# Kernel optimization log

Hardware: AMD Instinct MI355X
Metric: run time of the kernel (lower is better)

## Reference

```python
import jax, jax.numpy as jnp
import numpy as np

B, S, H = 8, 512, 768
NH, KVH, HD = 12, 4, 64
E, TOPK, IE = 8, 2, 1536
EPS = 1e-6
ROPE_THETA = 10000.0


def _rmsnorm(x, w):
    xf = x.astype(jnp.float32)
    var = jnp.mean(xf * xf, axis=-1, keepdims=True)
    return (w * (xf * jax.lax.rsqrt(var + EPS))).astype(x.dtype)


def _rotate_half(x):
    x1, x2 = jnp.split(x, 2, axis=-1)
    return jnp.concatenate((-x2, x1), axis=-1)


def setup_inputs() -> dict:
    key = jax.random.key(0)
    ks = iter(jax.random.split(key, 40))

    def nrm(shape, scale=0.02):
        return jax.random.normal(next(ks), shape, dtype=jnp.float32) * scale

    inp = {}
    inp["hidden_states"] = jax.random.normal(next(ks), (B, S, H), dtype=jnp.float32)
    causal = jnp.tril(jnp.ones((S, S), dtype=bool))
    inp["attention_mask"] = jnp.where(causal, 0.0, -1e9).astype(jnp.float32)[None, None]  # [1,1,S,S]
    inp["group_attention_mask"] = jnp.zeros((S, 1, B, B), dtype=jnp.float32)
    inp["position_ids"] = jnp.broadcast_to(jnp.arange(S, dtype=jnp.int32), (B, S))
    # RMSNorm weights
    inp["ln1_w"] = jnp.ones((H,), jnp.float32)
    inp["ln2_w"] = jnp.ones((H,), jnp.float32)
    inp["ln3_w"] = jnp.ones((H,), jnp.float32)
    # self (time) attention params
    inp["sq_w"] = nrm((NH * HD, H)); inp["sq_b"] = jnp.zeros((NH * HD,), jnp.float32)
    inp["sk_w"] = nrm((KVH * HD, H)); inp["sk_b"] = jnp.zeros((KVH * HD,), jnp.float32)
    inp["sv_w"] = nrm((KVH * HD, H)); inp["sv_b"] = jnp.zeros((KVH * HD,), jnp.float32)
    inp["so_w"] = nrm((H, NH * HD))
    # group (cross-channel) attention params
    inp["gq_w"] = nrm((NH * HD, H)); inp["gq_b"] = jnp.zeros((NH * HD,), jnp.float32)
    inp["gk_w"] = nrm((KVH * HD, H)); inp["gk_b"] = jnp.zeros((KVH * HD,), jnp.float32)
    inp["gv_w"] = nrm((KVH * HD, H)); inp["gv_b"] = jnp.zeros((KVH * HD,), jnp.float32)
    inp["go_w"] = nrm((H, NH * HD))
    # MoE params: router + stacked expert weights
    inp["gate_w"] = nrm((E, H))
    inp["w_gate"] = nrm((E, H, IE))
    inp["w_up"] = nrm((E, H, IE))
    inp["w_down"] = nrm((E, IE, H))
    return inp


def reference(hidden_states, attention_mask, group_attention_mask, position_ids,
              ln1_w, ln2_w, ln3_w,
              sq_w, sq_b, sk_w, sk_b, sv_w, sv_b, so_w,
              gq_w, gq_b, gk_w, gk_b, gv_w, gv_b, go_w,
              gate_w, w_gate, w_up, w_down):
    dtype = hidden_states.dtype
    b, s, h = hidden_states.shape
    rep = NH // KVH
    scale = 1.0 / np.sqrt(HD).astype(np.float32)

    # ---- self attention with RoPE (causal, GQA) ----
    residual = hidden_states
    x = _rmsnorm(hidden_states, ln1_w)
    q = (x @ sq_w.T + sq_b).reshape(b, s, NH, HD).transpose(0, 2, 1, 3)   # [b,n,s,d]
    k = (x @ sk_w.T + sk_b).reshape(b, s, KVH, HD).transpose(0, 2, 1, 3)
    v = (x @ sv_w.T + sv_b).reshape(b, s, KVH, HD).transpose(0, 2, 1, 3)
    inv_freq = 1.0 / (ROPE_THETA ** (jnp.arange(0, HD, 2, dtype=jnp.float32) / HD))
    freqs = position_ids.astype(jnp.float32)[..., None] * inv_freq        # [b,s,d/2]
    emb = jnp.concatenate((freqs, freqs), axis=-1)
    cos = jnp.cos(emb)[:, None].astype(dtype)                             # [b,1,s,d]
    sin = jnp.sin(emb)[:, None].astype(dtype)
    q = q * cos + _rotate_half(q) * sin
    k = k * cos + _rotate_half(k) * sin
    k = jnp.repeat(k, rep, axis=1)
    v = jnp.repeat(v, rep, axis=1)
    scores = jnp.einsum('bnqd,bnkd->bnqk', q, k) * scale + attention_mask
    probs = jax.nn.softmax(scores.astype(jnp.float32), axis=-1).astype(dtype)
    attn = jnp.einsum('bnqk,bnkd->bnqd', probs, v)
    attn = attn.transpose(0, 2, 1, 3).reshape(b, s, h) @ so_w.T
    hidden_states = residual + attn

    # ---- group attention: MHA across channels (batch dim), no RoPE ----
    residual = hidden_states
    xg = _rmsnorm(hidden_states, ln2_w).transpose(1, 0, 2)                # [s,b,h]
    q = (xg @ gq_w.T + gq_b).reshape(s, b, NH, HD).transpose(0, 2, 1, 3)  # [s,n,b,d]
    k = (xg @ gk_w.T + gk_b).reshape(s, b, KVH, HD).transpose(0, 2, 1, 3)
    v = (xg @ gv_w.T + gv_b).reshape(s, b, KVH, HD).transpose(0, 2, 1, 3)
    k = jnp.repeat(k, rep, axis=1)
    v = jnp.repeat(v, rep, axis=1)
    gsc = jnp.einsum('snbd,sncd->snbc', q, k) * scale + group_attention_mask
    gpr = jax.nn.softmax(gsc.astype(jnp.float32), axis=-1).astype(dtype)
    ga = jnp.einsum('snbc,sncd->snbd', gpr, v)                            # [s,n,b,d]
    ga = ga.transpose(0, 2, 1, 3).reshape(s, b, h) @ go_w.T               # [s,b,h]
    hidden_states = residual + ga.transpose(1, 0, 2)

    # ---- sparse MoE FFN (top-k routing, weights NOT renormalized) ----
    residual = hidden_states
    xf = _rmsnorm(hidden_states, ln3_w).reshape(b * s, h)                 # [T,h]
    logits = xf @ gate_w.T                                                # [T,E]
    routing = jax.nn.softmax(logits.astype(jnp.float32), axis=-1)
    topw, topi = jax.lax.top_k(routing, TOPK)
    combine = jnp.zeros((b * s, E), jnp.float32).at[
        jnp.arange(b * s)[:, None], topi].set(topw)                        # [T,E]
    out = jnp.zeros_like(xf)
    for e in range(E):  # fixed small expert count; each iter is a grouped GEMM
        ge = jax.nn.silu(xf @ w_gate[e]) * (xf @ w_up[e])                 # [T,IE]
        out = out + combine[:, e:e + 1].astype(dtype) * (ge @ w_down[e])
    hidden_states = residual + out.reshape(b, s, h)
    return hidden_states
```

## Files before the change

### kernel.cpp

```cpp
#include <hip/hip_runtime.h>
#include <math.h>

#define BATCH 8
#define SEQ 512
#define HID 768
#define NHEAD 12
#define KVHEAD 4
#define HDIM 64
#define NEXP 8
#define TOPK 2
#define IEXP 1536
#define NTOK (BATCH * SEQ)
#define NSLOT (NTOK * TOPK)
#define REP (NHEAD / KVHEAD)

typedef unsigned short u16;
typedef float f32x4 __attribute__((ext_vector_type(4)));
typedef __bf16 bf16x8 __attribute__((ext_vector_type(8)));
typedef unsigned short u16x8 __attribute__((ext_vector_type(8)));

__device__ __forceinline__ u16 f2bf(float f) {
    unsigned u = __float_as_uint(f);
    u += 0x7fffu + ((u >> 16) & 1u);
    return (u16)(u >> 16);
}
__device__ __forceinline__ float bf2f(u16 h) {
    return __uint_as_float(((unsigned)h) << 16);
}

__device__ __forceinline__ void gload16(const void* g, void* l) {
    __builtin_amdgcn_global_load_lds(
        (const __attribute__((address_space(1))) void*)g,
        (__attribute__((address_space(3))) void*)l, 16, 0, 0);
}

__device__ __forceinline__ void cvt8(float4 a, float4 b, u16x8& hi, u16x8& lo) {
    float x[8] = {a.x, a.y, a.z, a.w, b.x, b.y, b.z, b.w};
#pragma unroll
    for (int i = 0; i < 8; ++i) {
        u16 h = f2bf(x[i]);
        hi[i] = h;
        lo[i] = f2bf(x[i] - bf2f(h));
    }
}

#define SW(row, col) (((row) << 6) + ((col) ^ (((row) & 7) << 3)))

__global__ __launch_bounds__(256)
void cvt_split(const float* __restrict__ x, u16* __restrict__ yh,
               u16* __restrict__ yl, int n) {
    int i = (blockIdx.x * 256 + threadIdx.x) * 4;
    if (i >= n) return;
    float4 v = *(const float4*)(x + i);
    float a[4] = {v.x, v.y, v.z, v.w};
    ushort4 h, lo;
    u16 t;
    t = f2bf(a[0]); h.x = t; lo.x = f2bf(a[0] - bf2f(t));
    t = f2bf(a[1]); h.y = t; lo.y = f2bf(a[1] - bf2f(t));
    t = f2bf(a[2]); h.z = t; lo.z = f2bf(a[2] - bf2f(t));
    t = f2bf(a[3]); h.w = t; lo.w = f2bf(a[3] - bf2f(t));
    *(ushort4*)(yh + i) = h;
    *(ushort4*)(yl + i) = lo;
}

__global__ __launch_bounds__(256)
void transpose_cvt(const float* __restrict__ src, u16* __restrict__ dst,
                   int R, int C) {
    const int e = blockIdx.z;
    src += (size_t)e * R * C;
    dst += (size_t)e * R * C;
    __shared__ float t[32][33];
    const int c0 = blockIdx.x << 5, r0 = blockIdx.y << 5;
    const int tx = threadIdx.x, ty = threadIdx.y;
#pragma unroll
    for (int i = 0; i < 4; ++i)
        t[ty * 4 + i][tx] = src[(size_t)(r0 + ty * 4 + i) * C + c0 + tx];
    __syncthreads();
#pragma unroll
    for (int i = 0; i < 4; ++i)
        dst[(size_t)(c0 + ty * 4 + i) * R + r0 + tx] = f2bf(t[tx][ty * 4 + i]);
}

__global__ __launch_bounds__(256)
void rmsnorm_kernel(const float* __restrict__ X, const float* __restrict__ W,
                    float* __restrict__ Y) {
    const int t = blockIdx.x;
    const int tid = threadIdx.x;
    const float* x = X + (size_t)t * HID;
    float x0 = x[tid], x1 = x[tid + 256], x2 = x[tid + 512];
    float ss = x0 * x0 + x1 * x1 + x2 * x2;
    for (int m = 1; m < 64; m <<= 1) ss += __shfl_xor(ss, m);
    __shared__ float red[4];
    if ((tid & 63) == 0) red[tid >> 6] = ss;
    __syncthreads();
    float tot = red[0] + red[1] + red[2] + red[3];
    float inv = rsqrtf(tot * (1.0f / HID) + 1e-6f);
    float* y = Y + (size_t)t * HID;
    y[tid]       = x0 * inv * W[tid];
    y[tid + 256] = x1 * inv * W[tid + 256];
    y[tid + 512] = x2 * inv * W[tid + 512];
}

__global__ __launch_bounds__(256)
void qkv_split(const float* __restrict__ X, const u16* __restrict__ Wh,
               const u16* __restrict__ Wl,
               const float* __restrict__ bq, const float* __restrict__ bk,
               const float* __restrict__ bv,
               float* __restrict__ Qo, float* __restrict__ Ko,
               float* __restrict__ Vo) {
    __shared__ __align__(16) u16 Ah[4096], Al[4096], Bh[4096], Bl[4096];
    const int tid = threadIdx.x, l = tid & 63, w = tid >> 6;
    const int wm = w & 1, wn = w >> 1;
    const int m0 = blockIdx.y << 7, n0 = blockIdx.x << 7;
    const int sr = l >> 2, sc8 = (l & 3) << 3;
    const float* gA0 = X + (size_t)(m0 + w * 32 + sr) * HID + sc8;
    const float* gA1 = gA0 + 16 * HID;
    const u16* gBh0 = Wh + (size_t)(n0 + w * 32 + sr) * HID + sc8;
    const u16* gBh1 = gBh0 + 16 * HID;
    const u16* gBl0 = Wl + (size_t)(n0 + w * 32 + sr) * HID + sc8;
    const u16* gBl1 = gBl0 + 16 * HID;
    const int aoff0 = (w * 32 + sr) * 32 + sc8, aoff1 = aoff0 + 512;
    u16* lBh0 = Bh + w * 1024; u16* lBh1 = lBh0 + 512;
    u16* lBl0 = Bl + w * 1024; u16* lBl1 = lBl0 + 512;
    const int fr = l & 15, fc = (l >> 4) << 3;
    f32x4 acc[4][4];
#pragma unroll
    for (int i = 0; i < 4; ++i)
#pragma unroll
        for (int j = 0; j < 4; ++j) acc[i][j] = (f32x4){0.f, 0.f, 0.f, 0.f};
    for (int k0 = 0; k0 < HID; k0 += 32) {
        float4 a00 = *(const float4*)(gA0 + k0);
        float4 a01 = *(const float4*)(gA0 + k0 + 4);
        float4 a10 = *(const float4*)(gA1 + k0);
        float4 a11 = *(const float4*)(gA1 + k0 + 4);
        gload16(gBh0 + k0, lBh0);
        gload16(gBh1 + k0, lBh1);
        gload16(gBl0 + k0, lBl0);
        gload16(gBl1 + k0, lBl1);
        u16x8 h0, l0v, h1, l1v;
        cvt8(a00, a01, h0, l0v);
        cvt8(a10, a11, h1, l1v);
        *(u16x8*)(Ah + aoff0) = h0; *(u16x8*)(Al + aoff0) = l0v;
        *(u16x8*)(Ah + aoff1) = h1; *(u16x8*)(Al + aoff1) = l1v;
        __syncthreads();
        bf16x8 ah[4], al[4], bh[4], bl[4];
#pragma unroll
        for (int i = 0; i < 4; ++i) {
            ah[i] = *(const bf16x8*)(Ah + (wm * 64 + i * 16 + fr) * 32 + fc);
            al[i] = *(const bf16x8*)(Al + (wm * 64 + i * 16 + fr) * 32 + fc);
            bh[i] = *(const bf16x8*)(Bh + (wn * 64 + i * 16 + fr) * 32 + fc);
            bl[i] = *(const bf16x8*)(Bl + (wn * 64 + i * 16 + fr) * 32 + fc);
        }
#pragma unroll
        for (int mf = 0; mf < 4; ++mf)
#pragma unroll
            for (int nf = 0; nf < 4; ++nf) {
                acc[mf][nf] = __builtin_amdgcn_mfma_f32_16x16x32_bf16(
                    ah[mf], bh[nf], acc[mf][nf], 0, 0, 0);
                acc[mf][nf] = __builtin_amdgcn_mfma_f32_16x16x32_bf16(
                    al[mf], bh[nf], acc[mf][nf], 0, 0, 0);
                acc[mf][nf] = __builtin_amdgcn_mfma_f32_16x16x32_bf16(
                    ah[mf], bl[nf], acc[mf][nf], 0, 0, 0);
            }
        __syncthreads();
    }
    float* outp; const float* bp; int ldc, nl;
    if (n0 < 768)       { outp = Qo; bp = bq; ldc = 768; nl = n0; }
    else if (n0 < 1024) { outp = Ko; bp = bk; ldc = 256; nl = n0 - 768; }
    else                { outp = Vo; bp = bv; ldc = 256; nl = n0 - 1024; }
    const int er = (l >> 4) << 2, ec = l & 15;
#pragma unroll
    for (int mf = 0; mf < 4; ++mf)
#pragma unroll
        for (int i = 0; i < 4; ++i) {
            int row = m0 + wm * 64 + mf * 16 + er + i;
#pragma unroll
            for (int nf = 0; nf < 4; ++nf) {
                int col = nl + wn * 64 + nf * 16 + ec;
                outp[(size_t)row * ldc + col] = acc[mf][nf][i] + bp[col];
            }
        }
}

__global__ __launch_bounds__(256)
void oproj_split(const float* __restrict__ A, const u16* __restrict__ Wh,
                 const u16* __restrict__ Wl, const float* __restrict__ resid,
                 float* __restrict__ C, int M, int N, int K) {
    __shared__ __align__(16) u16 Ah[4096], Al[4096], Bh[4096], Bl[4096];
    const int tid = threadIdx.x, l = tid & 63, w = tid >> 6;
    const int wm = w & 1, wn = w >> 1;
    const int m0 = blockIdx.y << 7, n0 = blockIdx.x << 7;
    const int sr = l >> 2, sc8 = (l & 3) << 3;
    const float* gA0 = A + (size_t)(m0 + w * 32 + sr) * K + sc8;
    const float* gA1 = gA0 + (size_t)16 * K;
    const u16* gBh0 = Wh + (size_t)(n0 + w * 32 + sr) * K + sc8;
    const u16* gBh1 = gBh0 + (size_t)16 * K;
    const u16* gBl0 = Wl + (size_t)(n0 + w * 32 + sr) * K + sc8;
    const u16* gBl1 = gBl0 + (size_t)16 * K;
    const int aoff0 = (w * 32 + sr) * 32 + sc8, aoff1 = aoff0 + 512;
    u16* lBh0 = Bh + w * 1024; u16* lBh1 = lBh0 + 512;
    u16* lBl0 = Bl + w * 1024; u16* lBl1 = lBl0 + 512;
    const int fr = l & 15, fc = (l >> 4) << 3;
    f32x4 acc[4][4];
#pragma unroll
    for (int i = 0; i < 4; ++i)
#pragma unroll
        for (int j = 0; j < 4; ++j) acc[i][j] = (f32x4){0.f, 0.f, 0.f, 0.f};
    for (int k0 = 0; k0 < K; k0 += 32) {
        float4 a00 = *(const float4*)(gA0 + k0);
        float4 a01 = *(const float4*)(gA0 + k0 + 4);
        float4 a10 = *(const float4*)(gA1 + k0);
        float4 a11 = *(const float4*)(gA1 + k0 + 4);
        gload16(gBh0 + k0, lBh0);
        gload16(gBh1 + k0, lBh1);
        gload16(gBl0 + k0, lBl0);
        gload16(gBl1 + k0, lBl1);
        u16x8 h0, l0v, h1, l1v;
        cvt8(a00, a01, h0, l0v);
        cvt8(a10, a11, h1, l1v);
        *(u16x8*)(Ah + aoff0) = h0; *(u16x8*)(Al + aoff0) = l0v;
        *(u16x8*)(Ah + aoff1) = h1; *(u16x8*)(Al + aoff1) = l1v;
        __syncthreads();
        bf16x8 ah[4], al[4], bh[4], bl[4];
#pragma unroll
        for (int i = 0; i < 4; ++i) {
            ah[i] = *(const bf16x8*)(Ah + (wm * 64 + i * 16 + fr) * 32 + fc);
            al[i] = *(const bf16x8*)(Al + (wm * 64 + i * 16 + fr) * 32 + fc);
            bh[i] = *(const bf16x8*)(Bh + (wn * 64 + i * 16 + fr) * 32 + fc);
            bl[i] = *(const bf16x8*)(Bl + (wn * 64 + i * 16 + fr) * 32 + fc);
        }
#pragma unroll
        for (int mf = 0; mf < 4; ++mf)
#pragma unroll
            for (int nf = 0; nf < 4; ++nf) {
                acc[mf][nf] = __builtin_amdgcn_mfma_f32_16x16x32_bf16(
                    ah[mf], bh[nf], acc[mf][nf], 0, 0, 0);
                acc[mf][nf] = __builtin_amdgcn_mfma_f32_16x16x32_bf16(
                    al[mf], bh[nf], acc[mf][nf], 0, 0, 0);
                acc[mf][nf] = __builtin_amdgcn_mfma_f32_16x16x32_bf16(
                    ah[mf], bl[nf], acc[mf][nf], 0, 0, 0);
            }
        __syncthreads();
    }
    const int er = (l >> 4) << 2, ec = l & 15;
#pragma unroll
    for (int mf = 0; mf < 4; ++mf)
#pragma unroll
        for (int i = 0; i < 4; ++i) {
            int row = m0 + wm * 64 + mf * 16 + er + i;
#pragma unroll
            for (int nf = 0; nf < 4; ++nf) {
                int col = n0 + wn * 64 + nf * 16 + ec;
                C[(size_t)row * N + col] =
                    acc[mf][nf][i] + resid[(size_t)row * N + col];
            }
        }
}

__global__ __launch_bounds__(256)
void rope_kernel(float* __restrict__ Q, float* __restrict__ Kb,
                 const int* __restrict__ pos_ids) {
    const int t = blockIdx.x;
    const float pos = (float)pos_ids[t];
    const int tid = threadIdx.x;
#pragma unroll
    for (int it = 0; it < 2; ++it) {
        int p = tid + (it << 8);
        int head = p >> 5, i = p & 31;
        float invf = expf(-(float)i * 0.28782313662425572f);
        float ang = pos * invf;
        float c = cosf(ang), sn = sinf(ang);
        float* base = (head < NHEAD)
            ? (Q + (size_t)t * HID + head * HDIM)
            : (Kb + (size_t)t * (KVHEAD * HDIM) + (head - NHEAD) * HDIM);
        float x1 = base[i], x2 = base[i + 32];
        base[i]      = x1 * c - x2 * sn;
        base[i + 32] = x2 * c + x1 * sn;
    }
}

__global__ __launch_bounds__(256)
void attn_self_mfma(const float* __restrict__ Q, const float* __restrict__ K,
                    const float* __restrict__ V, float* __restrict__ O) {
    const int qt = blockIdx.x, n = blockIdx.y, b = blockIdx.z;
    const int kv = n / REP;
    const int tid = threadIdx.x, l = tid & 63, w = tid >> 6;
    const int q0 = qt << 5;
    __shared__ __align__(16) u16 Qh[2048], Ql[2048];
    __shared__ __align__(16) u16 Kh[4096], Kl[4096];
    __shared__ __align__(16) u16 Vh[4096], Vl[4096];
    __shared__ float Ps[32][68];
    __shared__ float scal[32];

    {
        int row = tid >> 3, cg = (tid & 7) << 3;
        const float* qg = Q + (size_t)(b * SEQ + q0 + row) * HID + n * HDIM + cg;
        float4 v0 = *(const float4*)qg;
        float4 v1 = *(const float4*)(qg + 4);
        u16x8 h, lo;
        cvt8(v0, v1, h, lo);
        *(u16x8*)(Qh + SW(row, cg)) = h;
        *(u16x8*)(Ql + SW(row, cg)) = lo;
    }
    __syncthreads();

    const int fr = l & 15, fcg = (l >> 4) << 3;
    const int qf16 = (w & 1) << 4;
    const int fp2 = (w >> 1) << 1;
    bf16x8 qfh[2], qfl[2];
#pragma unroll
    for (int dc = 0; dc < 2; ++dc) {
        int off = SW(qf16 + fr, dc * 32 + fcg);
        qfh[dc] = *(const bf16x8*)(Qh + off);
        qfl[dc] = *(const bf16x8*)(Ql + off);
    }

    f32x4 o[2];
    o[0] = (f32x4){0.f, 0.f, 0.f, 0.f};
    o[1] = (f32x4){0.f, 0.f, 0.f, 0.f};
    float m_run = -3.4e38f, l_run = 0.f;
    const int sq = tid >> 3;
    const int skb = (tid & 7) << 3;
    const float scale = 0.125f;
    const int nt = (qt >> 1) + 1;

    for (int t = 0; t < nt; ++t) {
        __syncthreads();
        {
            int row = tid >> 2, cg = (tid & 3) << 4;
            const float* kg = K + (size_t)(b * SEQ + (t << 6) + row)
                              * (KVHEAD * HDIM) + kv * HDIM + cg;
            float4 k0 = *(const float4*)kg;
            float4 k1 = *(const float4*)(kg + 4);
            float4 k2 = *(const float4*)(kg + 8);
            float4 k3 = *(const float4*)(kg + 12);
            u16x8 h0, l0v, h1, l1v;
            cvt8(k0, k1, h0, l0v);
            cvt8(k2, k3, h1, l1v);
            *(u16x8*)(Kh + SW(row, cg)) = h0;
            *(u16x8*)(Kh + SW(row, cg + 8)) = h1;
            *(u16x8*)(Kl + SW(row, cg)) = l0v;
            *(u16x8*)(Kl + SW(row, cg + 8)) = l1v;
        }
        {
            int kp = (tid & 31) << 1, dc = (tid >> 5) << 3;
            const float* vg0 = V + (size_t)(b * SEQ + (t << 6) + kp)
                               * (KVHEAD * HDIM) + kv * HDIM + dc;
            const float* vg1 = vg0 + KVHEAD * HDIM;
            float4 a0 = *(const float4*)vg0;
            float4 a1 = *(const float4*)(vg0 + 4);
            float4 b0 = *(const float4*)vg1;
            float4 b1 = *(const float4*)(vg1 + 4);
            float va[8] = {a0.x, a0.y, a0.z, a0.w, a1.x, a1.y, a1.z, a1.w};
            float vb[8] = {b0.x, b0.y, b0.z, b0.w, b1.x, b1.y, b1.z, b1.w};
#pragma unroll
            for (int j = 0; j < 8; ++j) {
                u16 h0 = f2bf(va[j]);
                u16 h1 = f2bf(vb[j]);
                u16 p0 = f2bf(va[j] - bf2f(h0));
                u16 p1 = f2bf(vb[j] - bf2f(h1));
                int off = SW(dc + j, kp);
                *(unsigned*)(Vh + off) = (unsigned)h0 | ((unsigned)h1 << 16);
                *(unsigned*)(Vl + off) = (unsigned)p0 | ((unsigned)p1 << 16);
            }
        }
        __syncthreads();
#pragma unroll
        for (int kk = 0; kk < 2; ++kk) {
            int kf = fp2 + kk;
            bf16x8 kh[2], klv[2];
#pragma unroll
            for (int dc = 0; dc < 2; ++dc) {
                int off = SW(kf * 16 + fr, dc * 32 + fcg);
                kh[dc]  = *(const bf16x8*)(Kh + off);
                klv[dc] = *(const bf16x8*)(Kl + off);
            }
            f32x4 s = (f32x4){0.f, 0.f, 0.f, 0.f};
            s = __builtin_amdgcn_mfma_f32_16x16x32_bf16(qfh[0], kh[0], s, 0, 0, 0);
            s = __builtin_amdgcn_mfma_f32_16x16x32_bf16(qfh[1], kh[1], s, 0, 0, 0);
            s = __builtin_amdgcn_mfma_f32_16x16x32_bf16(qfl[0], kh[0], s, 0, 0, 0);
            s = __builtin_amdgcn_mfma_f32_16x16x32_bf16(qfl[1], kh[1], s, 0, 0, 0);
            s = __builtin_amdgcn_mfma_f32_16x16x32_bf16(qfh[0], klv[0], s, 0, 0, 0);
            s = __builtin_amdgcn_mfma_f32_16x16x32_bf16(qfh[1], klv[1], s, 0, 0, 0);
            int col = kf * 16 + fr;
            int key = (t << 6) + col;
#pragma unroll
            for (int r = 0; r < 4; ++r) {
                int qrow = qf16 + ((l >> 4) << 2) + r;
                Ps[qrow][col] = (key <= q0 + qrow) ? s[r] * scale : -1e9f;
            }
        }
        __syncthreads();
        {
            float4 s0 = *(const float4*)&Ps[sq][skb];
            float4 s1 = *(const float4*)&Ps[sq][skb + 4];
            float sv[8] = {s0.x, s0.y, s0.z, s0.w, s1.x, s1.y, s1.z, s1.w};
            float mx = sv[0];
#pragma unroll
            for (int j = 1; j < 8; ++j) mx = fmaxf(mx, sv[j]);
            for (int x = 1; x < 8; x <<= 1) mx = fmaxf(mx, __shfl_xor(mx, x));
            float mnew = fmaxf(m_run, mx);
            float corr = __expf(m_run - mnew);
            float lsum = 0.f;
#pragma unroll
            for (int j = 0; j < 8; ++j) {
                sv[j] = __expf(sv[j] - mnew);
                lsum += sv[j];
            }
            for (int x = 1; x < 8; x <<= 1) lsum += __shfl_xor(lsum, x);
            l_run = l_run * corr + lsum;
            m_run = mnew;
            *(float4*)&Ps[sq][skb]     = make_float4(sv[0], sv[1], sv[2], sv[3]);
            *(float4*)&Ps[sq][skb + 4] = make_float4(sv[4], sv[5], sv[6], sv[7]);
            if ((tid & 7) == 0) scal[sq] = corr;
        }
        __syncthreads();
        {
            float4 c4 = *(const float4*)&scal[qf16 + ((l >> 4) << 2)];
            float cr[4] = {c4.x, c4.y, c4.z, c4.w};
#pragma unroll
            for (int dfi = 0; dfi < 2; ++dfi)
#pragma unroll
                for (int r = 0; r < 4; ++r) o[dfi][r] *= cr[r];
            bf16x8 ph[2], pl[2];
#pragma unroll
            for (int kc = 0; kc < 2; ++kc) {
                float4 p0 = *(const float4*)&Ps[qf16 + fr][kc * 32 + fcg];
                float4 p1 = *(const float4*)&Ps[qf16 + fr][kc * 32 + fcg + 4];
                u16x8 hh, ll;
                cvt8(p0, p1, hh, ll);
                ph[kc] = *(bf16x8*)&hh;
                pl[kc] = *(bf16x8*)&ll;
            }
#pragma unroll
            for (int dfi = 0; dfi < 2; ++dfi) {
                int df = fp2 + dfi;
#pragma unroll
                for (int kc = 0; kc < 2; ++kc) {
                    int off = SW(df * 16 + fr, kc * 32 + fcg);
                    bf16x8 vh = *(const bf16x8*)(Vh + off);
                    bf16x8 vl = *(const bf16x8*)(Vl + off);
                    o[dfi] = __builtin_amdgcn_mfma_f32_16x16x32_bf16(
                        ph[kc], vh, o[dfi], 0, 0, 0);
                    o[dfi] = __builtin_amdgcn_mfma_f32_16x16x32_bf16(
                        pl[kc], vh, o[dfi], 0, 0, 0);
                    o[dfi] = __builtin_amdgcn_mfma_f32_16x16x32_bf16(
                        ph[kc], vl, o[dfi], 0, 0, 0);
                }
            }
        }
    }
    __syncthreads();
    if ((tid & 7) == 0) scal[sq] = 1.0f / l_run;
    __syncthreads();
    {
        int qrb = qf16 + ((l >> 4) << 2);
        float4 li4 = *(const float4*)&scal[qrb];
        float li[4] = {li4.x, li4.y, li4.z, li4.w};
#pragma unroll
        for (int dfi = 0; dfi < 2; ++dfi) {
            int df = fp2 + dfi;
            int col = n * HDIM + df * 16 + fr;
#pragma unroll
            for (int r = 0; r < 4; ++r) {
                int row = q0 + qrb + r;
                O[(size_t)(b * SEQ + row) * HID + col] = o[dfi][r] * li[r];
            }
        }
    }
}

__global__ __launch_bounds__(64)
void attn_group(const float* __restrict__ Q, const float* __restrict__ K,
                const float* __restrict__ V, const float* __restrict__ gmask,
                float* __restrict__ O) {
    const int n = blockIdx.x % NHEAD;
    const int s = blockIdx.x / NHEAD;
    const int kv = n / REP;
    const int lane = threadIdx.x;
    __shared__ float Qs[8][65], Ks[8][65], Vs[8][65], Ps[64];
    for (int c = 0; c < 8; ++c) {
        Qs[c][lane] = Q[(size_t)(c * SEQ + s) * HID + n * HDIM + lane];
        Ks[c][lane] = K[(size_t)(c * SEQ + s) * (KVHEAD * HDIM) + kv * HDIM + lane];
        Vs[c][lane] = V[(size_t)(c * SEQ + s) * (KVHEAD * HDIM) + kv * HDIM + lane];
    }
    __syncthreads();
    const int qb = lane >> 3, kb = lane & 7;
    float sc = 0;
    for (int d = 0; d < 64; ++d) sc += Qs[qb][d] * Ks[kb][d];
    sc = sc * 0.125f + gmask[(size_t)s * 64 + qb * 8 + kb];
    float m = sc;
    for (int x = 1; x < 8; x <<= 1) m = fmaxf(m, __shfl_xor(m, x));
    float p = __expf(sc - m);
    float l = p;
    for (int x = 1; x < 8; x <<= 1) l += __shfl_xor(l, x);
    Ps[lane] = p / l;
    __syncthreads();
    for (int q2 = 0; q2 < 8; ++q2) {
        float o = 0;
        for (int c = 0; c < 8; ++c) o += Ps[q2 * 8 + c] * Vs[c][lane];
        O[(size_t)(q2 * SEQ + s) * HID + n * HDIM + lane] = o;
    }
}

__global__ __launch_bounds__(64)
void router_kernel(const float* __restrict__ X, const float* __restrict__ GW,
                   int* __restrict__ counts, int* __restrict__ topi,
                   float* __restrict__ topw, int* __restrict__ posb) {
    const int t = blockIdx.x;
    const int lane = threadIdx.x;
    const int e = lane >> 3, c = lane & 7;
    const float4* x4 = (const float4*)(X + (size_t)t * HID + c * 96);
    const float4* g4 = (const float4*)(GW + (size_t)e * HID + c * 96);
    float p = 0;
#pragma unroll
    for (int i = 0; i < 24; ++i) {
        float4 xv = x4[i], gv = g4[i];
        p += xv.x * gv.x + xv.y * gv.y + xv.z * gv.z + xv.w * gv.w;
    }
    p += __shfl_xor(p, 1);
    p += __shfl_xor(p, 2);
    p += __shfl_xor(p, 4);
    float lg[8];
#pragma unroll
    for (int i = 0; i < 8; ++i) lg[i] = __shfl(p, i * 8);
    float m = lg[0];
#pragma unroll
    for (int i = 1; i < 8; ++i) m = fmaxf(m, lg[i]);
    float s = 0;
#pragma unroll
    for (int i = 0; i < 8; ++i) { lg[i] = expf(lg[i] - m); s += lg[i]; }
    float inv = 1.0f / s;
    int i1 = 0; float b1 = lg[0];
#pragma unroll
    for (int i = 1; i < 8; ++i) if (lg[i] > b1) { b1 = lg[i]; i1 = i; }
    int i2 = -1; float b2 = -1.0f;
#pragma unroll
    for (int i = 0; i < 8; ++i)
        if (i != i1 && lg[i] > b2) { b2 = lg[i]; i2 = i; }
    if (lane == 0) {
        topi[t * 2] = i1; topi[t * 2 + 1] = i2;
        topw[t * 2] = b1 * inv; topw[t * 2 + 1] = b2 * inv;
        posb[t * 2] = atomicAdd(&counts[i1], 1);
        posb[t * 2 + 1] = atomicAdd(&counts[i2], 1);
    }
}

__global__ void scan_kernel(const int* __restrict__ counts, int* __restrict__ offsets) {
    int acc = 0;
    for (int e = 0; e < NEXP; ++e) { offsets[e] = acc; acc += counts[e]; }
}

__global__ __launch_bounds__(256)
void fill_slots(const int* __restrict__ topi, const float* __restrict__ topw,
                const int* __restrict__ posb, const int* __restrict__ offsets,
                int* __restrict__ slot_token, float* __restrict__ slot_w,
                int* __restrict__ token_slot) {
    int t = blockIdx.x * 256 + threadIdx.x;
    if (t >= NTOK) return;
#pragma unroll
    for (int k = 0; k < TOPK; ++k) {
        int e = topi[t * 2 + k];
        int sl = offsets[e] + posb[t * 2 + k];
        slot_token[sl] = t;
        slot_w[sl] = topw[t * 2 + k];
        token_slot[t * 2 + k] = sl;
    }
}

__global__ __launch_bounds__(256)
void moe_gate_up(const float* __restrict__ X, const u16* __restrict__ Wg,
                 const u16* __restrict__ Wu,
                 const int* __restrict__ slot_token,
                 const int* __restrict__ counts,
                 const int* __restrict__ offsets, u16* __restrict__ H) {
    const int e = blockIdx.z;
    const int Ce = counts[e];
    const int m0 = blockIdx.y << 7;
    if (Ce == 0 || m0 >= Ce) return;
    const int n0 = blockIdx.x << 7;
    const int base = offsets[e];
    __shared__ __align__(16) u16 Ah[4096];
    __shared__ __align__(16) u16 Al[4096];
    __shared__ __align__(16) u16 Gs[4096];
    __shared__ __align__(16) u16 Us[4096];
    const int tid = threadIdx.x, l = tid & 63, w = tid >> 6;
    const int wm = w & 1, wn = w >> 1;
    const int sr = l >> 2, sc8 = (l & 3) << 3;
    int r0 = m0 + w * 32 + sr;
    int r1 = r0 + 16;
    int t0 = slot_token[base + min(r0, Ce - 1)];
    int t1 = slot_token[base + min(r1, Ce - 1)];
    const float* gA0 = X + (size_t)t0 * HID + sc8;
    const float* gA1 = X + (size_t)t1 * HID + sc8;
    const u16* Wge = Wg + (size_t)e * IEXP * HID;
    const u16* Wue = Wu + (size_t)e * IEXP * HID;
    const u16* gG0 = Wge + (size_t)(n0 + w * 32 + sr) * HID + sc8;
    const u16* gG1 = gG0 + 16 * HID;
    const u16* gU0 = Wue + (size_t)(n0 + w * 32 + sr) * HID + sc8;
    const u16* gU1 = gU0 + 16 * HID;
    const int aoff0 = (w * 32 + sr) * 32 + sc8, aoff1 = aoff0 + 512;
    u16* lG0 = Gs + w * 1024; u16* lG1 = lG0 + 512;
    u16* lU0 = Us + w * 1024; u16* lU1 = lU0 + 512;
    const int fr = l & 15, fc = (l >> 4) << 3;
    f32x4 accg[4][4], accu[4][4];
#pragma unroll
    for (int i = 0; i < 4; ++i)
#pragma unroll
        for (int j = 0; j < 4; ++j) {
            accg[i][j] = (f32x4){0.f, 0.f, 0.f, 0.f};
            accu[i][j] = (f32x4){0.f, 0.f, 0.f, 0.f};
        }
    for (int k0 = 0; k0 < HID; k0 += 32) {
        float4 a00 = *(const float4*)(gA0 + k0);
        float4 a01 = *(const float4*)(gA0 + k0 + 4);
        float4 a10 = *(const float4*)(gA1 + k0);
        float4 a11 = *(const float4*)(gA1 + k0 + 4);
        gload16(gG0 + k0, lG0);
        gload16(gG1 + k0, lG1);
        gload16(gU0 + k0, lU0);
        gload16(gU1 + k0, lU1);
        u16x8 h0, lo0, h1, lo1;
        cvt8(a00, a01, h0, lo0);
        cvt8(a10, a11, h1, lo1);
        *(u16x8*)(Ah + aoff0) = h0; *(u16x8*)(Al + aoff0) = lo0;
        *(u16x8*)(Ah + aoff1) = h1; *(u16x8*)(Al + aoff1) = lo1;
        __syncthreads();
        bf16x8 ah[4], al[4], gf[4], uf[4];
#pragma unroll
        for (int i = 0; i < 4; ++i) {
            ah[i] = *(const bf16x8*)(Ah + (wm * 64 + i * 16 + fr) * 32 + fc);
            al[i] = *(const bf16x8*)(Al + (wm * 64 + i * 16 + fr) * 32 + fc);
            gf[i] = *(const bf16x8*)(Gs + (wn * 64 + i * 16 + fr) * 32 + fc);
            uf[i] = *(const bf16x8*)(Us + (wn * 64 + i * 16 + fr) * 32 + fc);
        }
#pragma unroll
        for (int mf = 0; mf < 4; ++mf)
#pragma unroll
            for (int nf = 0; nf < 4; ++nf) {
                accg[mf][nf] = __builtin_amdgcn_mfma_f32_16x16x32_bf16(
                    ah[mf], gf[nf], accg[mf][nf], 0, 0, 0);
                accg[mf][nf] = __builtin_amdgcn_mfma_f32_16x16x32_bf16(
                    al[mf], gf[nf], accg[mf][nf], 0, 0, 0);
                accu[mf][nf] = __builtin_amdgcn_mfma_f32_16x16x32_bf16(
                    ah[mf], uf[nf], accu[mf][nf], 0, 0, 0);
                accu[mf][nf] = __builtin_amdgcn_mfma_f32_16x16x32_bf16(
                    al[mf], uf[nf], accu[mf][nf], 0, 0, 0);
            }
        __syncthreads();
    }
    const int er = (l >> 4) << 2, ec = l & 15;
#pragma unroll
    for (int mf = 0; mf < 4; ++mf)
#pragma unroll
        for (int i = 0; i < 4; ++i) {
            int row = m0 + wm * 64 + mf * 16 + er + i;
            if (row >= Ce) continue;
            size_t sl = (size_t)(base + row);
#pragma unroll
            for (int nf = 0; nf < 4; ++nf) {
                int col = n0 + wn * 64 + nf * 16 + ec;
                float g = accg[mf][nf][i];
                float u = accu[mf][nf][i];
                float h = g / (1.0f + __expf(-g)) * u;
                H[sl * IEXP + col] = f2bf(h);
            }
        }
}

__global__ __launch_bounds__(256)
void moe_down_bf16(const u16* __restrict__ Hb, const u16* __restrict__ Wd,
                   const float* __restrict__ slot_w,
                   const int* __restrict__ counts,
                   const int* __restrict__ offsets, float* __restrict__ D) {
    const int e = blockIdx.z;
    const int Ce = counts[e];
    const int m0 = blockIdx.y << 7;
    if (Ce == 0 || m0 >= Ce) return;
    const int n0 = blockIdx.x << 7;
    const int base = offsets[e];
    __shared__ __align__(16) u16 As[4096];
    __shared__ __align__(16) u16 Bs[4096];
    const int tid = threadIdx.x, l = tid & 63, w = tid >> 6;
    const int wm = w & 1, wn = w >> 1;
    const int sr = l >> 2, sc = (l & 3) << 3;
    const u16* Ae = Hb + (size_t)base * IEXP;
    int r0 = min(m0 + w * 32 + sr, Ce - 1);
    int r1 = min(m0 + w * 32 + 16 + sr, Ce - 1);
    const u16* gA0 = Ae + (size_t)r0 * IEXP + sc;
    const u16* gA1 = Ae + (size_t)r1 * IEXP + sc;
    const u16* Wde = Wd + (size_t)e * HID * IEXP;
    const u16* gB0 = Wde + (size_t)(n0 + w * 32 + sr) * IEXP + sc;
    const u16* gB1 = gB0 + 16 * IEXP;
    u16* lA0 = As + w * 1024; u16* lA1 = lA0 + 512;
    u16* lB0 = Bs + w * 1024; u16* lB1 = lB0 + 512;
    const int fr = l & 15, fc = (l >> 4) << 3;
    f32x4 acc[4][4];
#pragma unroll
    for (int i = 0; i < 4; ++i)
#pragma unroll
        for (int j = 0; j < 4; ++j) acc[i][j] = (f32x4){0.f, 0.f, 0.f, 0.f};
    for (int k0 = 0; k0 < IEXP; k0 += 32) {
        gload16(gA0 + k0, lA0);
        gload16(gA1 + k0, lA1);
        gload16(gB0 + k0, lB0);
        gload16(gB1 + k0, lB1);
        __syncthreads();
        bf16x8 af[4], bfv[4];
#pragma unroll
        for (int i = 0; i < 4; ++i) {
            af[i]  = *(const bf16x8*)(As + (wm * 64 + i * 16 + fr) * 32 + fc);
            bfv[i] = *(const bf16x8*)(Bs + (wn * 64 + i * 16 + fr) * 32 + fc);
        }
#pragma unroll
        for (int mf = 0; mf < 4; ++mf)
#pragma unroll
            for (int nf = 0; nf < 4; ++nf)
                acc[mf][nf] = __builtin_amdgcn_mfma_f32_16x16x32_bf16(
                    af[mf], bfv[nf], acc[mf][nf], 0, 0, 0);
        __syncthreads();
    }
    const int er = (l >> 4) << 2, ec = l & 15;
#pragma unroll
    for (int mf = 0; mf < 4; ++mf)
#pragma unroll
        for (int i = 0; i < 4; ++i) {
            int row = m0 + wm * 64 + mf * 16 + er + i;
            if (row >= Ce) continue;
            size_t sl = (size_t)(base + row);
            float sw = slot_w[sl];
#pragma unroll
            for (int nf = 0; nf < 4; ++nf) {
                int col = n0 + wn * 64 + nf * 16 + ec;
                D[sl * HID + col] = acc[mf][nf][i] * sw;
            }
        }
}

__global__ __launch_bounds__(256)
void moe_add(float* __restrict__ out, const float* __restrict__ D,
             const int* __restrict__ token_slot) {
    const int t = blockIdx.y;
    const int h = blockIdx.x * 256 + threadIdx.x;
    int s0 = token_slot[t * 2], s1 = token_slot[t * 2 + 1];
    out[(size_t)t * HID + h] += D[(size_t)s0 * HID + h] + D[(size_t)s1 * HID + h];
}

extern "C" void kernel_launch(void* const* d_in, const int* in_sizes, int n_in,
                              void* d_out, int out_size, void* d_ws, size_t ws_size,
                              hipStream_t stream) {
    const float* hidden = (const float*)d_in[0];
    const float* amask  = (const float*)d_in[1];
    const float* gmask  = (const float*)d_in[2];
    const int*   posids = (const int*)d_in[3];
    const float* ln1 = (const float*)d_in[4];
    const float* ln2 = (const float*)d_in[5];
    const float* ln3 = (const float*)d_in[6];
    const float* sqw = (const float*)d_in[7];  const float* sqb = (const float*)d_in[8];
    const float* skw = (const float*)d_in[9];  const float* skb = (const float*)d_in[10];
    const float* svw = (const float*)d_in[11]; const float* svb = (const float*)d_in[12];
    const float* sow = (const float*)d_in[13];
    const float* gqw = (const float*)d_in[14]; const float* gqb = (const float*)d_in[15];
    const float* gkw = (const float*)d_in[16]; const float* gkb = (const float*)d_in[17];
    const float* gvw = (const float*)d_in[18]; const float* gvb = (const float*)d_in[19];
    const float* gow = (const float*)d_in[20];
    const float* gatew = (const float*)d_in[21];
    const float* wg = (const float*)d_in[22];
    const float* wu = (const float*)d_in[23];
    const float* wd = (const float*)d_in[24];
    float* out = (float*)d_out;
    (void)amask;

    char* base = (char*)d_ws;
    float* xb     = (float*)(base + 0);
    float* qb     = (float*)(base + 12582912);
    float* kbuf   = (float*)(base + 25165824);
    float* vbuf   = (float*)(base + 29360128);
    float* ab     = (float*)(base + 33554432);
    u16* wqkv_sh  = (u16*)(base + 46137344);
    u16* wqkv_sl  = (u16*)(base + 48103424);
    u16* wo_sh    = (u16*)(base + 50069504);
    u16* wo_sl    = (u16*)(base + 51249152);
    u16* wqkv_gh  = (u16*)(base + 52428800);
    u16* wqkv_gl  = (u16*)(base + 54394880);
    u16* wo_gh    = (u16*)(base + 56360960);
    u16* wo_gl    = (u16*)(base + 57540608);
    u16* wgt      = (u16*)(base + 58720256);
    u16* wut      = (u16*)(base + 77594624);
    u16* wdt      = (u16*)(base + 96468992);
    float* slotw  = (float*)(base + 115343360);
    float* topw   = (float*)(base + 115376128);
    int* counts   = (int*)(base + 115408896);
    int* offsets  = (int*)(base + 115409024);
    int* topi     = (int*)(base + 115409408);
    int* posb     = (int*)(base + 115442176);
    int* slot_token = (int*)(base + 115474944);
    int* token_slot = (int*)(base + 115507712);
    u16*   Hbuf  = (u16*)  (base + 12582912);
    float* Dbuf  = (float*)(base + 37748736);

    cvt_split<<<576, 256, 0, stream>>>(sqw, wqkv_sh, wqkv_sl, 589824);
    cvt_split<<<192, 256, 0, stream>>>(skw, wqkv_sh + 589824, wqkv_sl + 589824, 196608);
    cvt_split<<<192, 256, 0, stream>>>(svw, wqkv_sh + 786432, wqkv_sl + 786432, 196608);
    cvt_split<<<576, 256, 0, stream>>>(sow, wo_sh, wo_sl, 589824);
    cvt_split<<<576, 256, 0, stream>>>(gqw, wqkv_gh, wqkv_gl, 589824);
    cvt_split<<<192, 256, 0, stream>>>(gkw, wqkv_gh + 589824, wqkv_gl + 589824, 196608);
    cvt_split<<<192, 256, 0, stream>>>(gvw, wqkv_gh + 786432, wqkv_gl + 786432, 196608);
    cvt_split<<<576, 256, 0, stream>>>(gow, wo_gh, wo_gl, 589824);
    transpose_cvt<<<dim3(48, 24, 8), dim3(32, 8), 0, stream>>>(wg, wgt, HID, IEXP);
    transpose_cvt<<<dim3(48, 24, 8), dim3(32, 8), 0, stream>>>(wu, wut, HID, IEXP);
    transpose_cvt<<<dim3(24, 48, 8), dim3(32, 8), 0, stream>>>(wd, wdt, IEXP, HID);

    rmsnorm_kernel<<<NTOK, 256, 0, stream>>>(hidden, ln1, xb);
    qkv_split<<<dim3(10, 32), 256, 0, stream>>>(xb, wqkv_sh, wqkv_sl,
                                                sqb, skb, svb, qb, kbuf, vbuf);
    rope_kernel<<<NTOK, 256, 0, stream>>>(qb, kbuf, posids);
    attn_self_mfma<<<dim3(SEQ / 32, NHEAD, BATCH), 256, 0, stream>>>(qb, kbuf, vbuf, ab);
    oproj_split<<<dim3(6, 32), 256, 0, stream>>>(ab, wo_sh, wo_sl, hidden, out,
                                                 NTOK, HID, HID);

    rmsnorm_kernel<<<NTOK, 256, 0, stream>>>(out, ln2, xb);
    qkv_split<<<dim3(10, 32), 256, 0, stream>>>(xb, wqkv_gh, wqkv_gl,
                                                gqb, gkb, gvb, qb, kbuf, vbuf);
    attn_group<<<SEQ * NHEAD, 64, 0, stream>>>(qb, kbuf, vbuf, gmask, ab);
    oproj_split<<<dim3(6, 32), 256, 0, stream>>>(ab, wo_gh, wo_gl, out, out,
                                                 NTOK, HID, HID);

    rmsnorm_kernel<<<NTOK, 256, 0, stream>>>(out, ln3, xb);
    hipMemsetAsync(counts, 0, 8 * sizeof(int), stream);
    router_kernel<<<NTOK, 64, 0, stream>>>(xb, gatew, counts, topi, topw, posb);
    scan_kernel<<<1, 1, 0, stream>>>(counts, offsets);
    fill_slots<<<16, 256, 0, stream>>>(topi, topw, posb, offsets,
                                       slot_token, slotw, token_slot);
    moe_gate_up<<<dim3(12, 32, 8), 256, 0, stream>>>(
        xb, wgt, wut, slot_token, counts, offsets, Hbuf);
    moe_down_bf16<<<dim3(6, 32, 8), 256, 0, stream>>>(
        Hbuf, wdt, slotw, counts, offsets, Dbuf);
    moe_add<<<dim3(3, NTOK), 256, 0, stream>>>(out, Dbuf, token_slot);
}
```

Measured before the change: 676.8 us.

## Use single bf16 activations in MoE gate/up and swap grid axes

The final RMSNorm now also writes a bf16 copy of the normalized activations. The MoE gate/up GEMM loads this copy directly into LDS with gload16, replacing the fp32 load, hi/lo split conversion and doubled MFMA count. The error-compensating low half is dropped, which lowers accuracy relative to the split-bf16 path. The grid axes of both MoE GEMMs are also swapped so the token-tile index is the fastest-varying block coordinate, which changes block scheduling order and early-exit behaviour.

Measured after the change: 871.9 us. 28.8% more time.

```diff
diff --git a/kernel.cpp b/kernel.cpp
--- a/kernel.cpp
+++ b/kernel.cpp
@@ -83,7 +83,7 @@
 
 __global__ __launch_bounds__(256)
 void rmsnorm_kernel(const float* __restrict__ X, const float* __restrict__ W,
-                    float* __restrict__ Y) {
+                    float* __restrict__ Y, u16* __restrict__ Ybf) {
     const int t = blockIdx.x;
     const int tid = threadIdx.x;
     const float* x = X + (size_t)t * HID;
@@ -95,10 +95,15 @@
     __syncthreads();
     float tot = red[0] + red[1] + red[2] + red[3];
     float inv = rsqrtf(tot * (1.0f / HID) + 1e-6f);
+    float r0 = x0 * inv * W[tid];
+    float r1 = x1 * inv * W[tid + 256];
+    float r2 = x2 * inv * W[tid + 512];
     float* y = Y + (size_t)t * HID;
-    y[tid]       = x0 * inv * W[tid];
-    y[tid + 256] = x1 * inv * W[tid + 256];
-    y[tid + 512] = x2 * inv * W[tid + 512];
+    y[tid] = r0; y[tid + 256] = r1; y[tid + 512] = r2;
+    if (Ybf) {
+        u16* yb = Ybf + (size_t)t * HID;
+        yb[tid] = f2bf(r0); yb[tid + 256] = f2bf(r1); yb[tid + 512] = f2bf(r2);
+    }
 }
 
 __global__ __launch_bounds__(256)
@@ -569,19 +574,18 @@
 }
 
 __global__ __launch_bounds__(256)
-void moe_gate_up(const float* __restrict__ X, const u16* __restrict__ Wg,
+void moe_gate_up(const u16* __restrict__ Xb, const u16* __restrict__ Wg,
                  const u16* __restrict__ Wu,
                  const int* __restrict__ slot_token,
                  const int* __restrict__ counts,
                  const int* __restrict__ offsets, u16* __restrict__ H) {
     const int e = blockIdx.z;
     const int Ce = counts[e];
-    const int m0 = blockIdx.y << 7;
+    const int m0 = blockIdx.x << 7;
     if (Ce == 0 || m0 >= Ce) return;
-    const int n0 = blockIdx.x << 7;
+    const int n0 = blockIdx.y << 7;
     const int base = offsets[e];
-    __shared__ __align__(16) u16 Ah[4096];
-    __shared__ __align__(16) u16 Al[4096];
+    __shared__ __align__(16) u16 As[4096];
     __shared__ __align__(16) u16 Gs[4096];
     __shared__ __align__(16) u16 Us[4096];
     const int tid = threadIdx.x, l = tid & 63, w = tid >> 6;
@@ -591,15 +595,15 @@
     int r1 = r0 + 16;
     int t0 = slot_token[base + min(r0, Ce - 1)];
     int t1 = slot_token[base + min(r1, Ce - 1)];
-    const float* gA0 = X + (size_t)t0 * HID + sc8;
-    const float* gA1 = X + (size_t)t1 * HID + sc8;
+    const u16* gA0 = Xb + (size_t)t0 * HID + sc8;
+    const u16* gA1 = Xb + (size_t)t1 * HID + sc8;
     const u16* Wge = Wg + (size_t)e * IEXP * HID;
     const u16* Wue = Wu + (size_t)e * IEXP * HID;
     const u16* gG0 = Wge + (size_t)(n0 + w * 32 + sr) * HID + sc8;
     const u16* gG1 = gG0 + 16 * HID;
     const u16* gU0 = Wue + (size_t)(n0 + w * 32 + sr) * HID + sc8;
     const u16* gU1 = gU0 + 16 * HID;
-    const int aoff0 = (w * 32 + sr) * 32 + sc8, aoff1 = aoff0 + 512;
+    u16* lA0 = As + w * 1024; u16* lA1 = lA0 + 512;
     u16* lG0 = Gs + w * 1024; u16* lG1 = lG0 + 512;
     u16* lU0 = Us + w * 1024; u16* lU1 = lU0 + 512;
     const int fr = l & 15, fc = (l >> 4) << 3;
@@ -612,25 +616,17 @@
             accu[i][j] = (f32x4){0.f, 0.f, 0.f, 0.f};
         }
     for (int k0 = 0; k0 < HID; k0 += 32) {
-        float4 a00 = *(const float4*)(gA0 + k0);
-        float4 a01 = *(const float4*)(gA0 + k0 + 4);
-        float4 a10 = *(const float4*)(gA1 + k0);
-        float4 a11 = *(const float4*)(gA1 + k0 + 4);
+        gload16(gA0 + k0, lA0);
+        gload16(gA1 + k0, lA1);
         gload16(gG0 + k0, lG0);
         gload16(gG1 + k0, lG1);
         gload16(gU0 + k0, lU0);
         gload16(gU1 + k0, lU1);
-        u16x8 h0, lo0, h1, lo1;
-        cvt8(a00, a01, h0, lo0);
-        cvt8(a10, a11, h1, lo1);
-        *(u16x8*)(Ah + aoff0) = h0; *(u16x8*)(Al + aoff0) = lo0;
-        *(u16x8*)(Ah + aoff1) = h1; *(u16x8*)(Al + aoff1) = lo1;
-        __syncthreads();
-        bf16x8 ah[4], al[4], gf[4], uf[4];
+        __syncthreads();
+        bf16x8 af[4], gf[4], uf[4];
 #pragma unroll
         for (int i = 0; i < 4; ++i) {
-            ah[i] = *(const bf16x8*)(Ah + (wm * 64 + i * 16 + fr) * 32 + fc);
-            al[i] = *(const bf16x8*)(Al + (wm * 64 + i * 16 + fr) * 32 + fc);
+            af[i] = *(const bf16x8*)(As + (wm * 64 + i * 16 + fr) * 32 + fc);
             gf[i] = *(const bf16x8*)(Gs + (wn * 64 + i * 16 + fr) * 32 + fc);
             uf[i] = *(const bf16x8*)(Us + (wn * 64 + i * 16 + fr) * 32 + fc);
         }
@@ -639,13 +635,9 @@
 #pragma unroll
             for (int nf = 0; nf < 4; ++nf) {
                 accg[mf][nf] = __builtin_amdgcn_mfma_f32_16x16x32_bf16(
-                    ah[mf], gf[nf], accg[mf][nf], 0, 0, 0);
-                accg[mf][nf] = __builtin_amdgcn_mfma_f32_16x16x32_bf16(
-                    al[mf], gf[nf], accg[mf][nf], 0, 0, 0);
+                    af[mf], gf[nf], accg[mf][nf], 0, 0, 0);
                 accu[mf][nf] = __builtin_amdgcn_mfma_f32_16x16x32_bf16(
-                    ah[mf], uf[nf], accu[mf][nf], 0, 0, 0);
-                accu[mf][nf] = __builtin_amdgcn_mfma_f32_16x16x32_bf16(
-                    al[mf], uf[nf], accu[mf][nf], 0, 0, 0);
+                    af[mf], uf[nf], accu[mf][nf], 0, 0, 0);
             }
         __syncthreads();
     }
@@ -675,9 +667,9 @@
                    const int* __restrict__ offsets, float* __restrict__ D) {
     const int e = blockIdx.z;
     const int Ce = counts[e];
-    const int m0 = blockIdx.y << 7;
+    const int m0 = blockIdx.x << 7;
     if (Ce == 0 || m0 >= Ce) return;
-    const int n0 = blockIdx.x << 7;
+    const int n0 = blockIdx.y << 7;
     const int base = offsets[e];
     __shared__ __align__(16) u16 As[4096];
     __shared__ __align__(16) u16 Bs[4096];
@@ -796,6 +788,7 @@
     int* posb     = (int*)(base + 115442176);
     int* slot_token = (int*)(base + 115474944);
     int* token_slot = (int*)(base + 115507712);
+    u16* xbf      = (u16*)(base + 115540480);
     u16*   Hbuf  = (u16*)  (base + 12582912);
     float* Dbuf  = (float*)(base + 37748736);
 
@@ -811,7 +804,7 @@
     transpose_cvt<<<dim3(48, 24, 8), dim3(32, 8), 0, stream>>>(wu, wut, HID, IEXP);
     transpose_cvt<<<dim3(24, 48, 8), dim3(32, 8), 0, stream>>>(wd, wdt, IEXP, HID);
 
-    rmsnorm_kernel<<<NTOK, 256, 0, stream>>>(hidden, ln1, xb);
+    rmsnorm_kernel<<<NTOK, 256, 0, stream>>>(hidden, ln1, xb, nullptr);
     qkv_split<<<dim3(10, 32), 256, 0, stream>>>(xb, wqkv_sh, wqkv_sl,
                                                 sqb, skb, svb, qb, kbuf, vbuf);
     rope_kernel<<<NTOK, 256, 0, stream>>>(qb, kbuf, posids);
@@ -819,22 +812,22 @@
     oproj_split<<<dim3(6, 32), 256, 0, stream>>>(ab, wo_sh, wo_sl, hidden, out,
                                                  NTOK, HID, HID);
 
-    rmsnorm_kernel<<<NTOK, 256, 0, stream>>>(out, ln2, xb);
+    rmsnorm_kernel<<<NTOK, 256, 0, stream>>>(out, ln2, xb, nullptr);
     qkv_split<<<dim3(10, 32), 256, 0, stream>>>(xb, wqkv_gh, wqkv_gl,
                                                 gqb, gkb, gvb, qb, kbuf, vbuf);
     attn_group<<<SEQ * NHEAD, 64, 0, stream>>>(qb, kbuf, vbuf, gmask, ab);
     oproj_split<<<dim3(6, 32), 256, 0, stream>>>(ab, wo_gh, wo_gl, out, out,
                                                  NTOK, HID, HID);
 
-    rmsnorm_kernel<<<NTOK, 256, 0, stream>>>(out, ln3, xb);
+    rmsnorm_kernel<<<NTOK, 256, 0, stream>>>(out, ln3, xb, xbf);
     hipMemsetAsync(counts, 0, 8 * sizeof(int), stream);
     router_kernel<<<NTOK, 64, 0, stream>>>(xb, gatew, counts, topi, topw, posb);
     scan_kernel<<<1, 1, 0, stream>>>(counts, offsets);
     fill_slots<<<16, 256, 0, stream>>>(topi, topw, posb, offsets,
                                        slot_token, slotw, token_slot);
-    moe_gate_up<<<dim3(12, 32, 8), 256, 0, stream>>>(
-        xb, wgt, wut, slot_token, counts, offsets, Hbuf);
-    moe_down_bf16<<<dim3(6, 32, 8), 256, 0, stream>>>(
+    moe_gate_up<<<dim3(32, 12, 8), 256, 0, stream>>>(
+        xbf, wgt, wut, slot_token, counts, offsets, Hbuf);
+    moe_down_bf16<<<dim3(32, 6, 8), 256, 0, stream>>>(
         Hbuf, wdt, slotw, counts, offsets, Dbuf);
     moe_add<<<dim3(3, NTOK), 256, 0, stream>>>(out, Dbuf, token_slot);
 }
```
